# Performance work log

Hardware: AMD Instinct MI355X
Metric: run time of the kernel (lower is better)

The kernel has to match this reference:

```python
import jax, jax.numpy as jnp
import numpy as np

NC, NQ, BOX = 20, 27, 6  # classes, queries-per-class, 3D box dim (cx,cy,cz,w,h,d)
COST_CLASS, COST_BBOX, COST_GIOU = 2.0, 5.0, 2.0


def box_cxcyczwhd_to_xyzxyz(b):
    c, s = b[..., :3], b[..., 3:]
    return jnp.concatenate([c - 0.5 * s, c + 0.5 * s], axis=-1)


def giou3d_vs_single(pred, tgt):
    # pred: [B,NC,NQ,6] xyzxyz, tgt: [B,NC,6] xyzxyz -> giou [B,NC,NQ]
    vol_p = jnp.prod(pred[..., 3:] - pred[..., :3], -1)            # [B,NC,NQ]
    vol_t = jnp.prod(tgt[..., 3:] - tgt[..., :3], -1)[..., None]   # [B,NC,1]
    t = tgt[..., None, :]                                          # [B,NC,1,6]
    lt = jnp.maximum(pred[..., :3], t[..., :3])
    rb = jnp.minimum(pred[..., 3:], t[..., 3:])
    inter = jnp.prod(jnp.clip(rb - lt, 0.0), -1)                   # [B,NC,NQ]
    union = vol_p + vol_t - inter
    iou = inter / union
    lt2 = jnp.minimum(pred[..., :3], t[..., :3])
    rb2 = jnp.maximum(pred[..., 3:], t[..., 3:])
    hull = jnp.prod(jnp.clip(rb2 - lt2, 0.0), -1)
    return iou - (hull - union) / hull


def setup_inputs() -> dict:
    key = jax.random.key(0)
    k1, k2, k3, k4 = jax.random.split(key, 4)
    bs = 8192
    return {
        "pred_logits": jax.random.normal(k1, (bs, NC * NQ, 1), dtype=jnp.float32),
        "pred_boxes": jax.random.uniform(k2, (bs, NC * NQ, BOX), dtype=jnp.float32),
        "tgt_boxes": jax.random.uniform(k3, (bs, NC, BOX), dtype=jnp.float32),
        "tgt_present": jax.random.randint(k4, (bs, NC), 0, 2, dtype=jnp.int32),
        "num_top_queries": 1,
    }


def reference(pred_logits, pred_boxes, tgt_boxes, tgt_present, num_top_queries):
    bs = pred_logits.shape[0]
    boxes = pred_boxes.reshape(bs, NC, NQ, BOX).astype(jnp.float32)
    logits = pred_logits.reshape(bs, NC, NQ).astype(jnp.float32)

    cost_class = -jax.nn.sigmoid(logits)                                   # [B,NC,NQ]
    cost_bbox = jnp.sum(jnp.abs(boxes - tgt_boxes[:, :, None, :]), -1)      # L1 cdist, [B,NC,NQ]
    giou = giou3d_vs_single(box_cxcyczwhd_to_xyzxyz(jnp.clip(boxes, 0.0)),
                            box_cxcyczwhd_to_xyzxyz(tgt_boxes))
    cost_giou = -giou                                                       # [B,NC,NQ]

    C = COST_BBOX * cost_bbox + COST_CLASS * cost_class + COST_GIOU * cost_giou

    _, idx = jax.lax.top_k(-C, num_top_queries)                             # smallest-k, [B,NC,k]
    onehot = jax.nn.one_hot(idx, NQ, dtype=jnp.int32).sum(-2)               # [B,NC,NQ]
    present = tgt_present.astype(bool)[..., None]                           # [B,NC,1]
    matches = jnp.where(present, (onehot > 0).astype(jnp.int32), 0)

    gmax = cost_giou.max(-1, keepdims=True)
    gmin = cost_giou.min(-1, keepdims=True)
    soft = jnp.clip((cost_giou - gmax) / (gmin - gmax), 0.0)
    soft_labels = jnp.where(present, soft, -1.0)
    return matches, soft_labels
```

## Files before the change

kernel.cpp:

```cpp
#include <hip/hip_runtime.h>
#include <hip/hip_bf16.h>
#include <math.h>

#define NCC 20
#define NQQ 27
#define BSZ 8192
#define NPAIR (BSZ * NCC)

__device__ __forceinline__ float frcp(float x) { return __builtin_amdgcn_rcpf(x); }

struct Tgt {
    float tc0, tc1, tc2, tw, th, td;
    float tl0, tl1, tl2, th0, th1, th2, vol;
};

__device__ __forceinline__ Tgt make_tgt(float2 t01, float2 t23, float2 t45) {
    Tgt T;
    T.tc0 = t01.x; T.tc1 = t01.y; T.tc2 = t23.x;
    T.tw  = t23.y; T.th  = t45.x; T.td  = t45.y;
    T.tl0 = T.tc0 - 0.5f * T.tw; T.tl1 = T.tc1 - 0.5f * T.th; T.tl2 = T.tc2 - 0.5f * T.td;
    T.th0 = T.tc0 + 0.5f * T.tw; T.th1 = T.tc1 + 0.5f * T.th; T.th2 = T.tc2 + 0.5f * T.td;
    T.vol = (T.th0 - T.tl0) * (T.th1 - T.tl1) * (T.th2 - T.tl2);
    return T;
}

__device__ __forceinline__ float pair_cost(float2 b01, float2 b23, float2 b45,
                                           float lg, const Tgt& T, float* cg) {
    const float bc0 = b01.x, bc1 = b01.y, bc2 = b23.x;
    const float bw  = b23.y, bh  = b45.x, bd  = b45.y;

    const float cost_class = -frcp(1.0f + __expf(-lg));

    const float cost_bbox =
        fabsf(bc0 - T.tc0) + fabsf(bc1 - T.tc1) + fabsf(bc2 - T.tc2) +
        fabsf(bw  - T.tw ) + fabsf(bh  - T.th ) + fabsf(bd  - T.td );

    const float cc0 = fmaxf(bc0, 0.0f), cc1 = fmaxf(bc1, 0.0f), cc2 = fmaxf(bc2, 0.0f);
    const float cw  = fmaxf(bw , 0.0f), ch  = fmaxf(bh , 0.0f), cd  = fmaxf(bd , 0.0f);
    const float pl0 = cc0 - 0.5f * cw, pl1 = cc1 - 0.5f * ch, pl2 = cc2 - 0.5f * cd;
    const float ph0 = cc0 + 0.5f * cw, ph1 = cc1 + 0.5f * ch, ph2 = cc2 + 0.5f * cd;
    const float vol_p = (ph0 - pl0) * (ph1 - pl1) * (ph2 - pl2);

    const float i0 = fmaxf(fminf(ph0, T.th0) - fmaxf(pl0, T.tl0), 0.0f);
    const float i1 = fmaxf(fminf(ph1, T.th1) - fmaxf(pl1, T.tl1), 0.0f);
    const float i2 = fmaxf(fminf(ph2, T.th2) - fmaxf(pl2, T.tl2), 0.0f);
    const float inter = i0 * i1 * i2;
    const float uni   = vol_p + T.vol - inter;
    const float iou   = inter * frcp(uni);

    const float h0 = fmaxf(fmaxf(ph0, T.th0) - fminf(pl0, T.tl0), 0.0f);
    const float h1 = fmaxf(fmaxf(ph1, T.th1) - fminf(pl1, T.tl1), 0.0f);
    const float h2 = fmaxf(fmaxf(ph2, T.th2) - fminf(pl2, T.tl2), 0.0f);
    const float hull = h0 * h1 * h2;

    const float giou = iou - (hull - uni) * frcp(hull);
    *cg = -giou;
    return 5.0f * cost_bbox + 2.0f * cost_class + 2.0f * (-giou);
}

__global__ __launch_bounds__(256, 8) void matcher_kernel(
    const float* __restrict__ logits,
    const float* __restrict__ boxes,
    const float* __restrict__ tboxes,
    const int*   __restrict__ present,
    float* __restrict__ out_matches,
    float* __restrict__ out_soft)
{
    const int tid = blockIdx.x * blockDim.x + threadIdx.x;
    const int p   = tid >> 3;
    const int l   = tid & 7;
    const int q0  = l * 4;

    const int qa = (q0 + 0 < NQQ) ? q0 + 0 : NQQ - 1;
    const int qb = (q0 + 1 < NQQ) ? q0 + 1 : NQQ - 1;
    const int qc = (q0 + 2 < NQQ) ? q0 + 2 : NQQ - 1;
    const int qd = (q0 + 3 < NQQ) ? q0 + 3 : NQQ - 1;

    const float* bp = boxes + (size_t)p * (NQQ * 6);
    float2 a01 = *reinterpret_cast<const float2*>(bp + qa * 6 + 0);
    float2 a23 = *reinterpret_cast<const float2*>(bp + qa * 6 + 2);
    float2 a45 = *reinterpret_cast<const float2*>(bp + qa * 6 + 4);
    float2 b01 = *reinterpret_cast<const float2*>(bp + qb * 6 + 0);
    float2 b23 = *reinterpret_cast<const float2*>(bp + qb * 6 + 2);
    float2 b45 = *reinterpret_cast<const float2*>(bp + qb * 6 + 4);
    float2 c01 = *reinterpret_cast<const float2*>(bp + qc * 6 + 0);
    float2 c23 = *reinterpret_cast<const float2*>(bp + qc * 6 + 2);
    float2 c45 = *reinterpret_cast<const float2*>(bp + qc * 6 + 4);
    float2 d01 = *reinterpret_cast<const float2*>(bp + qd * 6 + 0);
    float2 d23 = *reinterpret_cast<const float2*>(bp + qd * 6 + 2);
    float2 d45 = *reinterpret_cast<const float2*>(bp + qd * 6 + 4);
    const float* lp = logits + (size_t)p * NQQ;
    const float lga = lp[qa], lgb = lp[qb], lgc = lp[qc], lgd = lp[qd];
    const float* t = tboxes + (size_t)p * 6;
    float2 t01 = *reinterpret_cast<const float2*>(t + 0);
    float2 t23 = *reinterpret_cast<const float2*>(t + 2);
    float2 t45 = *reinterpret_cast<const float2*>(t + 4);
    const int pres = present[p];

    const Tgt T = make_tgt(t01, t23, t45);

    const bool va = (q0 + 0 < NQQ), vb = (q0 + 1 < NQQ),
               vc = (q0 + 2 < NQQ), vd = (q0 + 3 < NQQ);

    float cg0, cg1, cg2, cg3;
    float C0 = pair_cost(a01, a23, a45, lga, T, &cg0);
    float C1 = pair_cost(b01, b23, b45, lgb, T, &cg1);
    float C2 = pair_cost(c01, c23, c45, lgc, T, &cg2);
    float C3 = pair_cost(d01, d23, d45, lgd, T, &cg3);
    if (!va) C0 = INFINITY;
    if (!vb) C1 = INFINITY;
    if (!vc) C2 = INFINITY;
    if (!vd) C3 = INFINITY;

    float bestC = C0; int bestj = 0;
    if (C1 < bestC) { bestC = C1; bestj = 1; }
    if (C2 < bestC) { bestC = C2; bestj = 2; }
    if (C3 < bestC) { bestC = C3; bestj = 3; }
    float gx = va ? cg0 : -INFINITY;
    float gn = va ? cg0 :  INFINITY;
    if (vb) { gx = fmaxf(gx, cg1); gn = fminf(gn, cg1); }
    if (vc) { gx = fmaxf(gx, cg2); gn = fminf(gn, cg2); }
    if (vd) { gx = fmaxf(gx, cg3); gn = fminf(gn, cg3); }

    float m = bestC;
#pragma unroll
    for (int s = 4; s >= 1; s >>= 1) {
        m  = fminf(m,  __shfl_xor(m,  s, 8));
        gx = fmaxf(gx, __shfl_xor(gx, s, 8));
        gn = fminf(gn, __shfl_xor(gn, s, 8));
    }

    const unsigned long long bal = __ballot(bestC == m);
    const int gbase  = (threadIdx.x & 63) & ~7;
    const unsigned int gbits = (unsigned int)(bal >> gbase) & 0xFFu;
    const int winner = __ffs(gbits) - 1;
    const bool mine  = (winner == l);

    float* om = out_matches + (size_t)p * NQQ + q0;
    float* os = out_soft    + (size_t)p * NQQ + q0;
    const float inv = frcp(gn - gx);
    if (va) { om[0] = (pres && mine && bestj == 0) ? 1.0f : 0.0f;
              os[0] = pres ? fmaxf((cg0 - gx) * inv, 0.0f) : -1.0f; }
    if (vb) { om[1] = (pres && mine && bestj == 1) ? 1.0f : 0.0f;
              os[1] = pres ? fmaxf((cg1 - gx) * inv, 0.0f) : -1.0f; }
    if (vc) { om[2] = (pres && mine && bestj == 2) ? 1.0f : 0.0f;
              os[2] = pres ? fmaxf((cg2 - gx) * inv, 0.0f) : -1.0f; }
    if (vd) { om[3] = (pres && mine && bestj == 3) ? 1.0f : 0.0f;
              os[3] = pres ? fmaxf((cg3 - gx) * inv, 0.0f) : -1.0f; }
}

extern "C" void kernel_launch(void* const* d_in, const int* in_sizes, int n_in,
                              void* d_out, int out_size, void* d_ws, size_t ws_size,
                              hipStream_t stream) {
    const float* logits  = (const float*)d_in[0];
    const float* boxes   = (const float*)d_in[1];
    const float* tboxes  = (const float*)d_in[2];
    const int*   presnt  = (const int*)d_in[3];

    float* out = (float*)d_out;
    float* out_matches = out;
    float* out_soft    = out + (size_t)NPAIR * NQQ;

    dim3 block(256);
    dim3 grid((NPAIR * 8) / 256);
    matcher_kernel<<<grid, block, 0, stream>>>(logits, boxes, tboxes, presnt,
                                               out_matches, out_soft);
}
```

Baseline: 34.89 us.

## Stage per-block inputs into LDS with coalesced float4 loads

Each block now cooperatively copies the boxes, logits, targets and present flags for its 32 pairs into shared memory using contiguous float4 loads, then computes from LDS. This replaces the strided per-thread global float2 loads, which were poorly coalesced because each pair spans 162 floats. It adds about 25 KB of LDS per block plus a barrier, and lowers the launch-bounds occupancy hint from 8 to 6.

```diff
diff --git a/kernel.cpp b/kernel.cpp
--- a/kernel.cpp
+++ b/kernel.cpp
@@ -6,6 +6,7 @@
 #define NQQ 27
 #define BSZ 8192
 #define NPAIR (BSZ * NCC)
+#define PPB 32
 
 __device__ __forceinline__ float frcp(float x) { return __builtin_amdgcn_rcpf(x); }
 
@@ -58,7 +59,7 @@
     return 5.0f * cost_bbox + 2.0f * cost_class + 2.0f * (-giou);
 }
 
-__global__ __launch_bounds__(256, 8) void matcher_kernel(
+__global__ __launch_bounds__(256, 6) void matcher_kernel(
     const float* __restrict__ logits,
     const float* __restrict__ boxes,
     const float* __restrict__ tboxes,
@@ -66,17 +67,40 @@
     float* __restrict__ out_matches,
     float* __restrict__ out_soft)
 {
-    const int tid = blockIdx.x * blockDim.x + threadIdx.x;
-    const int p   = tid >> 3;
-    const int l   = tid & 7;
-    const int q0  = l * 4;
+    __shared__ float sBox[PPB * 162];
+    __shared__ float sLog[PPB * NQQ];
+    __shared__ float sTgt[PPB * 6];
+    __shared__ int   sPres[PPB];
+
+    const int tid = threadIdx.x;
+    const size_t pairBase = (size_t)blockIdx.x * PPB;
+
+    {
+        const float4* srcB = reinterpret_cast<const float4*>(boxes + pairBase * 162);
+        float4* dstB = reinterpret_cast<float4*>(sBox);
+#pragma unroll
+        for (int i = 0; i < 5; ++i) dstB[i * 256 + tid] = srcB[i * 256 + tid];
+        if (tid < 16) dstB[1280 + tid] = srcB[1280 + tid];
+
+        if (tid < 216) reinterpret_cast<float4*>(sLog)[tid] =
+            reinterpret_cast<const float4*>(logits + pairBase * NQQ)[tid];
+        if (tid < 48)  reinterpret_cast<float4*>(sTgt)[tid] =
+            reinterpret_cast<const float4*>(tboxes + pairBase * 6)[tid];
+        if (tid < PPB) sPres[tid] = present[pairBase + tid];
+    }
+    __syncthreads();
+
+    const int lp = tid >> 3;
+    const int l  = tid & 7;
+    const int q0 = l * 4;
+    const size_t p = pairBase + lp;
 
     const int qa = (q0 + 0 < NQQ) ? q0 + 0 : NQQ - 1;
     const int qb = (q0 + 1 < NQQ) ? q0 + 1 : NQQ - 1;
     const int qc = (q0 + 2 < NQQ) ? q0 + 2 : NQQ - 1;
     const int qd = (q0 + 3 < NQQ) ? q0 + 3 : NQQ - 1;
 
-    const float* bp = boxes + (size_t)p * (NQQ * 6);
+    const float* bp = sBox + lp * 162;
     float2 a01 = *reinterpret_cast<const float2*>(bp + qa * 6 + 0);
     float2 a23 = *reinterpret_cast<const float2*>(bp + qa * 6 + 2);
     float2 a45 = *reinterpret_cast<const float2*>(bp + qa * 6 + 4);
@@ -89,13 +113,13 @@
     float2 d01 = *reinterpret_cast<const float2*>(bp + qd * 6 + 0);
     float2 d23 = *reinterpret_cast<const float2*>(bp + qd * 6 + 2);
     float2 d45 = *reinterpret_cast<const float2*>(bp + qd * 6 + 4);
-    const float* lp = logits + (size_t)p * NQQ;
-    const float lga = lp[qa], lgb = lp[qb], lgc = lp[qc], lgd = lp[qd];
-    const float* t = tboxes + (size_t)p * 6;
-    float2 t01 = *reinterpret_cast<const float2*>(t + 0);
-    float2 t23 = *reinterpret_cast<const float2*>(t + 2);
-    float2 t45 = *reinterpret_cast<const float2*>(t + 4);
-    const int pres = present[p];
+    const float* lpg = sLog + lp * NQQ;
+    const float lga = lpg[qa], lgb = lpg[qb], lgc = lpg[qc], lgd = lpg[qd];
+    const float* tp = sTgt + lp * 6;
+    float2 t01 = *reinterpret_cast<const float2*>(tp + 0);
+    float2 t23 = *reinterpret_cast<const float2*>(tp + 2);
+    float2 t45 = *reinterpret_cast<const float2*>(tp + 4);
+    const int pres = sPres[lp];
 
     const Tgt T = make_tgt(t01, t23, t45);
 
@@ -131,13 +155,13 @@
     }
 
     const unsigned long long bal = __ballot(bestC == m);
-    const int gbase  = (threadIdx.x & 63) & ~7;
+    const int gbase  = (tid & 63) & ~7;
     const unsigned int gbits = (unsigned int)(bal >> gbase) & 0xFFu;
     const int winner = __ffs(gbits) - 1;
     const bool mine  = (winner == l);
 
-    float* om = out_matches + (size_t)p * NQQ + q0;
-    float* os = out_soft    + (size_t)p * NQQ + q0;
+    float* om = out_matches + p * NQQ + q0;
+    float* os = out_soft    + p * NQQ + q0;
     const float inv = frcp(gn - gx);
     if (va) { om[0] = (pres && mine && bestj == 0) ? 1.0f : 0.0f;
               os[0] = pres ? fmaxf((cg0 - gx) * inv, 0.0f) : -1.0f; }
@@ -162,7 +186,7 @@
     float* out_soft    = out + (size_t)NPAIR * NQQ;
 
     dim3 block(256);
-    dim3 grid((NPAIR * 8) / 256);
+    dim3 grid(NPAIR / PPB);
     matcher_kernel<<<grid, block, 0, stream>>>(logits, boxes, tboxes, presnt,
                                                out_matches, out_soft);
 }
```

Measured after the change: 33.47 us. 1.04x faster.
